# Performance work log

Measured on AMD Instinct MI355X. Metric: run time of the kernel, lower is better.

The kernel has to match this reference:

```python
import jax, jax.numpy as jnp
import numpy as np

B, N = 256, 128000

def setup_inputs() -> dict:
    key = jax.random.key(0)
    k1, k2, k3 = jax.random.split(key, 3)
    logits = jax.random.normal(k1, (B, N), dtype=jnp.float32) * 4.0
    k = jax.random.randint(k2, (B,), 1, 1000, dtype=jnp.int32)
    p = jax.random.uniform(k3, (B,), dtype=jnp.float32, minval=0.05, maxval=0.99)
    return {"logits": logits, "k": k, "p": p}


def reference(logits, k, p):
    """Faithful jax version of original_apply_top_k_top_p (k and p both given).
    Sort ascending, mask everything below the k-th largest, then mask the
    low-probability prefix whose cumulative softmax mass is <= 1-p, and
    scatter the masked sorted logits back to original positions."""
    Bn, Nn = logits.shape
    k = jnp.clip(k, 1, Nn)
    idx = jnp.argsort(logits, axis=-1)                       # ascending order
    logits_sort = jnp.take_along_axis(logits, idx, axis=-1)
    neg_inf = jnp.float32(-jnp.inf)

    # --- top-k: threshold = value at position (N - k) in ascending order ---
    kth_pos = (Nn - k).astype(jnp.int32)[:, None]            # [B,1]
    kth_val = jnp.take_along_axis(logits_sort, kth_pos, axis=-1)
    logits_sort = jnp.where(logits_sort < kth_val, neg_inf, logits_sort)

    # --- top-p on the (top-k masked) sorted logits ---
    probs = jax.nn.softmax(logits_sort, axis=-1)
    probs_sum = jnp.cumsum(probs, axis=-1)
    top_p_mask = probs_sum <= (1.0 - p)[:, None]
    top_p_mask = top_p_mask.at[:, -1].set(False)             # always keep argmax
    logits_sort = jnp.where(top_p_mask, neg_inf, logits_sort)

    # --- scatter back to original vocabulary positions ---
    rows = jnp.arange(Bn)[:, None]
    out = jnp.empty_like(logits).at[rows, idx].set(logits_sort)
    return out
```

## Files before the change

### kernel.cpp

```cpp
#include <hip/hip_runtime.h>
#include <stdint.h>
#include <math.h>

#define BB 256
#define NN 128000
#define N4 (NN / 4)
#define CAP 2048
#define BLK 1024
#define THRESH 9.0f
#define LBUF_CAP 512
#define CHUNKS_PER_ROW 25
#define CHUNK_F4 (N4 / CHUNKS_PER_ROW)
#define MASK_BITS 0xFF7F0000u
#define BF16_FINITE_LIM 3.0e38f

#define CTR_STRIDE 4
#define WS_NEEDED ((size_t)4096 + (size_t)BB * CAP * sizeof(uint2))

typedef float f4v __attribute__((ext_vector_type(4)));

__device__ __forceinline__ uint32_t fkey_enc(uint32_t bits) {
  return (bits & 0x80000000u) ? ~bits : (bits | 0x80000000u);
}
__device__ __forceinline__ float fkey_dec(uint32_t fkey) {
  uint32_t bits = (fkey & 0x80000000u) ? (fkey ^ 0x80000000u) : ~fkey;
  return __uint_as_float(bits);
}

__global__ void k0_zero(uint32_t* counters) {
  int t = threadIdx.x;
  if (t < BB * CTR_STRIDE) counters[t] = 0u;
}

__global__ __launch_bounds__(256) void kGather(
    const float* __restrict__ logits, uint32_t* __restrict__ counters,
    uint2* __restrict__ pairs) {
  const int row = blockIdx.y;
  __shared__ uint2 lbuf[LBUF_CAP];
  __shared__ uint32_t lcount;
  __shared__ uint32_t gbase;
  if (threadIdx.x == 0) lcount = 0u;
  __syncthreads();

  const int t = (int)threadIdx.x;
  const int base = (int)blockIdx.x * CHUNK_F4;
  const f4v* in4 = (const f4v*)(logits + (size_t)row * NN);
  const f4v* a0 = in4 + (base + t);
  const f4v* a1 = in4 + (base + t + 256);
  const f4v* a2 = in4 + (base + t + 512);
  const f4v* a3 = in4 + (base + t + 768);
  const f4v* a4 = in4 + (base + t + 1024);

  f4v v0, v1, v2, v3, v4;
  asm volatile(
      "global_load_dwordx4 %0, %5, off\n\t"
      "global_load_dwordx4 %1, %6, off\n\t"
      "global_load_dwordx4 %2, %7, off\n\t"
      "global_load_dwordx4 %3, %8, off\n\t"
      "global_load_dwordx4 %4, %9, off\n\t"
      "s_waitcnt vmcnt(0)"
      : "=&v"(v0), "=&v"(v1), "=&v"(v2), "=&v"(v3), "=&v"(v4)
      : "v"(a0), "v"(a1), "v"(a2), "v"(a3), "v"(a4)
      : "memory");
  __builtin_amdgcn_sched_barrier(0);

#define PUSHC(x, colexpr)                                            \
  do {                                                               \
    if ((x) > THRESH) {                                              \
      uint32_t slot = atomicAdd(&lcount, 1u);                        \
      if (slot < LBUF_CAP)                                           \
        lbuf[slot] = make_uint2(fkey_enc(__float_as_uint(x)),        \
                                (uint32_t)(colexpr));                \
    }                                                                \
  } while (0)
#define CONSUME4(vv, fbase)                                          \
  do {                                                               \
    PUSHC((vv).x, (fbase) * 4 + 0);                                  \
    PUSHC((vv).y, (fbase) * 4 + 1);                                  \
    PUSHC((vv).z, (fbase) * 4 + 2);                                  \
    PUSHC((vv).w, (fbase) * 4 + 3);                                  \
  } while (0)
  CONSUME4(v0, base + t);
  CONSUME4(v1, base + t + 256);
  CONSUME4(v2, base + t + 512);
  CONSUME4(v3, base + t + 768);
  CONSUME4(v4, base + t + 1024);
#undef CONSUME4
#undef PUSHC
  __syncthreads();

  uint32_t n = lcount;
  if (threadIdx.x == 0) {
    if (n > LBUF_CAP) {
      atomicAdd(&counters[(size_t)row * CTR_STRIDE], (uint32_t)(CAP + 1));
      gbase = 0xFFFFFFFFu;
    } else {
      gbase = atomicAdd(&counters[(size_t)row * CTR_STRIDE], n);
    }
  }
  __syncthreads();
  uint32_t gb = gbase;
  if (gb == 0xFFFFFFFFu) return;
  for (uint32_t i = threadIdx.x; i < n; i += 256) {
    uint32_t s = gb + i;
    if (s < CAP) pairs[(size_t)row * CAP + s] = lbuf[i];
  }
}

__global__ __launch_bounds__(BLK) void kB_finalize(
    const float* __restrict__ logits, const int* __restrict__ kin,
    const float* __restrict__ pin, const uint32_t* __restrict__ counters,
    const uint2* __restrict__ pairs, float* __restrict__ out) {
  const int row = blockIdx.x;
  const int tid = threadIdx.x;

  __shared__ unsigned long long skey[CAP];
  __shared__ double dbuf[2][BLK];
  __shared__ uint32_t red[BLK];
  __shared__ uint32_t scount;

  {
    const float MASKV = __uint_as_float(MASK_BITS);
    const f4v mask4 = {MASKV, MASKV, MASKV, MASKV};
    f4v* out4 = (f4v*)(out + (size_t)row * NN);
    for (int i = tid; i < N4; i += BLK) out4[i] = mask4;
  }

  int k = kin[row];
  if (k < 1) k = 1;
  if (k > NN) k = NN;
  uint32_t c = counters[(size_t)row * CTR_STRIDE];

  if (c <= CAP && c >= (uint32_t)k) {
    for (int i = tid; i < (int)c; i += BLK) {
      uint2 pr = pairs[(size_t)row * CAP + i];
      skey[i] = ((unsigned long long)pr.x << 32) | (unsigned long long)pr.y;
    }
  } else {
    const float* rowp = logits + (size_t)row * NN;
    uint32_t lo = 0u, hi = 0xFFFFFFFFu;
    while (lo < hi) {
      uint32_t mid = (uint32_t)(((uint64_t)lo + (uint64_t)hi + 1ull) >> 1);
      uint32_t cnt = 0;
      for (int i = tid; i < NN; i += BLK)
        cnt += (fkey_enc(__float_as_uint(rowp[i])) >= mid) ? 1u : 0u;
      red[tid] = cnt;
      __syncthreads();
      for (int off = BLK / 2; off > 0; off >>= 1) {
        if (tid < off) red[tid] += red[tid + off];
        __syncthreads();
      }
      uint32_t total = red[0];
      __syncthreads();
      if (total >= (uint32_t)k) lo = mid;
      else hi = mid - 1u;
    }
    if (tid == 0) scount = 0u;
    __syncthreads();
    for (int i = tid; i < NN; i += BLK) {
      uint32_t fk = fkey_enc(__float_as_uint(rowp[i]));
      if (fk >= lo) {
        uint32_t slot = atomicAdd(&scount, 1u);
        if (slot < CAP) skey[slot] = ((unsigned long long)fk << 32) | (uint32_t)i;
      }
    }
    __syncthreads();
    c = scount;
    if (c > CAP) c = CAP;
  }
  if (c == 0u) return;
  if ((uint32_t)k > c) k = (int)c;

  for (int i = (int)c + tid; i < CAP; i += BLK) skey[i] = 0ull;
  __syncthreads();
  for (int kk = 2; kk <= CAP; kk <<= 1) {
    for (int j = kk >> 1; j > 0; j >>= 1) {
      for (int i = tid; i < CAP; i += BLK) {
        int ixj = i ^ j;
        if (ixj > i) {
          unsigned long long a = skey[i], b = skey[ixj];
          bool up = ((i & kk) == 0);
          if (up ? (a > b) : (a < b)) {
            skey[i] = b;
            skey[ixj] = a;
          }
        }
      }
      __syncthreads();
    }
  }

  const uint32_t mfkey = (uint32_t)(skey[CAP - 1] >> 32);
  const uint32_t kthfkey = (uint32_t)(skey[CAP - k] >> 32);
  const double mval = (double)fkey_dec(mfkey);
  const int base = CAP - (int)c;
  const float p = pin[row];
  const double lim_frac = (double)(1.0f - p);

  double loc[2];
  double chunk = 0.0;
#pragma unroll
  for (int j = 0; j < 2; ++j) {
    int i = tid * 2 + j;
    double e = 0.0;
    if (i >= base) {
      uint32_t fk = (uint32_t)(skey[i] >> 32);
      if (fk >= kthfkey) e = exp((double)fkey_dec(fk) - mval);
    }
    chunk += e;
    loc[j] = chunk;
  }
  dbuf[0][tid] = chunk;
  __syncthreads();
  int src = 0;
  for (int off = 1; off < BLK; off <<= 1) {
    double v = dbuf[src][tid];
    if (tid >= off) v += dbuf[src][tid - off];
    dbuf[src ^ 1][tid] = v;
    src ^= 1;
    __syncthreads();
  }
  const double S = dbuf[src][BLK - 1];
  const double lim = lim_frac * S;
  const double excl = (tid == 0) ? 0.0 : dbuf[src][tid - 1];

#pragma unroll
  for (int j = 0; j < 2; ++j) {
    int i = tid * 2 + j;
    if (i >= base) {
      unsigned long long sk = skey[i];
      uint32_t fk = (uint32_t)(sk >> 32);
      if (fk >= kthfkey) {
        double A = excl + loc[j];
        if (A > lim) {
          uint32_t col = (uint32_t)(sk & 0xFFFFFFFFull);
          float v = fkey_dec(fk);
          if (col < NN && isfinite(v) && fabsf(v) < BF16_FINITE_LIM)
            out[(size_t)row * NN + col] = v;
        }
      }
    }
  }
}

__global__ __launch_bounds__(BLK) void topk_topp_row(
    const float* __restrict__ logits, const int* __restrict__ kin,
    const float* __restrict__ pin, float* __restrict__ out) {
  const int row = blockIdx.x;
  const int tid = threadIdx.x;
  __shared__ unsigned long long skey[CAP];
  __shared__ double dbuf[2][BLK];
  __shared__ uint32_t red[BLK];
  __shared__ uint32_t scount;
  if (tid == 0) scount = 0u;
  __syncthreads();
  const float MASKV = __uint_as_float(MASK_BITS);
  const float4 mask4 = make_float4(MASKV, MASKV, MASKV, MASKV);
  const float4* in4 = (const float4*)(logits + (size_t)row * NN);
  float4* out4 = (float4*)(out + (size_t)row * NN);
  for (int c4 = tid; c4 < N4; c4 += BLK) {
    float4 v = in4[c4];
    out4[c4] = mask4;
    float vals[4] = {v.x, v.y, v.z, v.w};
#pragma unroll
    for (int j = 0; j < 4; ++j) {
      if (vals[j] > THRESH) {
        uint32_t slot = atomicAdd(&scount, 1u);
        if (slot < CAP)
          skey[slot] = ((unsigned long long)fkey_enc(__float_as_uint(vals[j])) << 32) |
                       (unsigned long long)(uint32_t)(c4 * 4 + j);
      }
    }
  }
  __syncthreads();
  int k = kin[row];
  if (k < 1) k = 1;
  if (k > NN) k = NN;
  uint32_t c = scount;
  if (c > CAP || c < (uint32_t)k) {
    const float* rowp = logits + (size_t)row * NN;
    uint32_t lo = 0u, hi = 0xFFFFFFFFu;
    while (lo < hi) {
      uint32_t mid = (uint32_t)(((uint64_t)lo + (uint64_t)hi + 1ull) >> 1);
      uint32_t cnt = 0;
      for (int i = tid; i < NN; i += BLK)
        cnt += (fkey_enc(__float_as_uint(rowp[i])) >= mid) ? 1u : 0u;
      red[tid] = cnt;
      __syncthreads();
      for (int off = BLK / 2; off > 0; off >>= 1) {
        if (tid < off) red[tid] += red[tid + off];
        __syncthreads();
      }
      uint32_t total = red[0];
      __syncthreads();
      if (total >= (uint32_t)k) lo = mid;
      else hi = mid - 1u;
    }
    if (tid == 0) scount = 0u;
    __syncthreads();
    for (int i = tid; i < NN; i += BLK) {
      uint32_t fk = fkey_enc(__float_as_uint(rowp[i]));
      if (fk >= lo) {
        uint32_t slot = atomicAdd(&scount, 1u);
        if (slot < CAP) skey[slot] = ((unsigned long long)fk << 32) | (uint32_t)i;
      }
    }
    __syncthreads();
    c = scount;
    if (c > CAP) c = CAP;
  }
  if (c == 0u) return;
  if ((uint32_t)k > c) k = (int)c;
  for (int i = (int)c + tid; i < CAP; i += BLK) skey[i] = 0ull;
  __syncthreads();
  for (int kk = 2; kk <= CAP; kk <<= 1) {
    for (int j = kk >> 1; j > 0; j >>= 1) {
      for (int i = tid; i < CAP; i += BLK) {
        int ixj = i ^ j;
        if (ixj > i) {
          unsigned long long a = skey[i], b = skey[ixj];
          bool up = ((i & kk) == 0);
          if (up ? (a > b) : (a < b)) {
            skey[i] = b;
            skey[ixj] = a;
          }
        }
      }
      __syncthreads();
    }
  }
  const uint32_t mfkey = (uint32_t)(skey[CAP - 1] >> 32);
  const uint32_t kthfkey = (uint32_t)(skey[CAP - k] >> 32);
  const double mval = (double)fkey_dec(mfkey);
  const int base = CAP - (int)c;
  const float p = pin[row];
  const double lim_frac = (double)(1.0f - p);
  double loc[2];
  double chunk = 0.0;
#pragma unroll
  for (int j = 0; j < 2; ++j) {
    int i = tid * 2 + j;
    double e = 0.0;
    if (i >= base) {
      uint32_t fk = (uint32_t)(skey[i] >> 32);
      if (fk >= kthfkey) e = exp((double)fkey_dec(fk) - mval);
    }
    chunk += e;
    loc[j] = chunk;
  }
  dbuf[0][tid] = chunk;
  __syncthreads();
  int src = 0;
  for (int off = 1; off < BLK; off <<= 1) {
    double v = dbuf[src][tid];
    if (tid >= off) v += dbuf[src][tid - off];
    dbuf[src ^ 1][tid] = v;
    src ^= 1;
    __syncthreads();
  }
  const double S = dbuf[src][BLK - 1];
  const double lim = lim_frac * S;
  const double excl = (tid == 0) ? 0.0 : dbuf[src][tid - 1];
#pragma unroll
  for (int j = 0; j < 2; ++j) {
    int i = tid * 2 + j;
    if (i >= base) {
      unsigned long long sk = skey[i];
      uint32_t fk = (uint32_t)(sk >> 32);
      if (fk >= kthfkey) {
        double A = excl + loc[j];
        if (A > lim) {
          uint32_t col = (uint32_t)(sk & 0xFFFFFFFFull);
          float v = fkey_dec(fk);
          if (col < NN && isfinite(v) && fabsf(v) < BF16_FINITE_LIM)
            out[(size_t)row * NN + col] = v;
        }
      }
    }
  }
}

extern "C" void kernel_launch(void* const* d_in, const int* in_sizes, int n_in,
                              void* d_out, int out_size, void* d_ws, size_t ws_size,
                              hipStream_t stream) {
  const float* logits = (const float*)d_in[0];
  const int* kk = (const int*)d_in[1];
  const float* pp = (const float*)d_in[2];
  float* out = (float*)d_out;
  (void)in_sizes; (void)n_in; (void)out_size;

  if (ws_size >= WS_NEEDED) {
    uint32_t* counters = (uint32_t*)d_ws;
    uint2* pairs = (uint2*)((char*)d_ws + 4096);
    k0_zero<<<1, 1024, 0, stream>>>(counters);
    dim3 gG(CHUNKS_PER_ROW, BB);
    kGather<<<gG, 256, 0, stream>>>(logits, counters, pairs);
    kB_finalize<<<BB, BLK, 0, stream>>>(logits, kk, pp, counters, pairs, out);
  } else {
    topk_topp_row<<<BB, BLK, 0, stream>>>(logits, kk, pp, out);
  }
}
```

Measured before the change: 83.59 us.

## Move output mask fill into gather kernel as interleaved fill blocks

The gather kernel now also launches fill blocks, one after every four gather blocks, and these write the masked default value over the whole output. The finalize kernel no longer fills its own row first. The aim is to overlap the output write traffic with the input read traffic in a single launch, instead of serializing the fill at the start of each finalize block. The cost is a larger combined grid and a finalize kernel that now depends on the fill having finished in the previous launch, which stream order guarantees. Finalize's fallback paths still write only the kept entries, so they rely on this fill.

```diff
diff --git a/kernel.cpp b/kernel.cpp
--- a/kernel.cpp
+++ b/kernel.cpp
@@ -11,6 +11,9 @@
 #define LBUF_CAP 512
 #define CHUNKS_PER_ROW 25
 #define CHUNK_F4 (N4 / CHUNKS_PER_ROW)
+#define GATHER_BLOCKS (BB * CHUNKS_PER_ROW)
+#define FILL_BLOCKS 1600
+#define FILL_F4 ((BB * N4) / FILL_BLOCKS)
 #define MASK_BITS 0xFF7F0000u
 #define BF16_FINITE_LIM 3.0e38f
 
@@ -32,18 +35,33 @@
   if (t < BB * CTR_STRIDE) counters[t] = 0u;
 }
 
-__global__ __launch_bounds__(256) void kGather(
-    const float* __restrict__ logits, uint32_t* __restrict__ counters,
-    uint2* __restrict__ pairs) {
-  const int row = blockIdx.y;
+__global__ __launch_bounds__(256) void kStream(
+    const float* __restrict__ logits, float* __restrict__ out,
+    uint32_t* __restrict__ counters, uint2* __restrict__ pairs) {
+  const int group = (int)blockIdx.x / 5;
+  const int within = (int)blockIdx.x % 5;
+  const int t = (int)threadIdx.x;
+
+  if (within == 4) {
+    const float MASKV = __uint_as_float(MASK_BITS);
+    const f4v mask4 = {MASKV, MASKV, MASKV, MASKV};
+    f4v* out4 = (f4v*)out;
+    const int s = group * FILL_F4;
+#pragma unroll 4
+    for (int i = s + t; i < s + FILL_F4; i += 256) out4[i] = mask4;
+    return;
+  }
+
+  const int gi = group * 4 + within;
+  const int row = gi / CHUNKS_PER_ROW;
+  const int base = (gi % CHUNKS_PER_ROW) * CHUNK_F4;
+
   __shared__ uint2 lbuf[LBUF_CAP];
   __shared__ uint32_t lcount;
   __shared__ uint32_t gbase;
-  if (threadIdx.x == 0) lcount = 0u;
-  __syncthreads();
-
-  const int t = (int)threadIdx.x;
-  const int base = (int)blockIdx.x * CHUNK_F4;
+  if (t == 0) lcount = 0u;
+  __syncthreads();
+
   const f4v* in4 = (const f4v*)(logits + (size_t)row * NN);
   const f4v* a0 = in4 + (base + t);
   const f4v* a1 = in4 + (base + t + 256);
@@ -90,7 +108,7 @@
   __syncthreads();
 
   uint32_t n = lcount;
-  if (threadIdx.x == 0) {
+  if (t == 0) {
     if (n > LBUF_CAP) {
       atomicAdd(&counters[(size_t)row * CTR_STRIDE], (uint32_t)(CAP + 1));
       gbase = 0xFFFFFFFFu;
@@ -101,7 +119,7 @@
   __syncthreads();
   uint32_t gb = gbase;
   if (gb == 0xFFFFFFFFu) return;
-  for (uint32_t i = threadIdx.x; i < n; i += 256) {
+  for (uint32_t i = (uint32_t)t; i < n; i += 256) {
     uint32_t s = gb + i;
     if (s < CAP) pairs[(size_t)row * CAP + s] = lbuf[i];
   }
@@ -118,13 +136,6 @@
   __shared__ double dbuf[2][BLK];
   __shared__ uint32_t red[BLK];
   __shared__ uint32_t scount;
-
-  {
-    const float MASKV = __uint_as_float(MASK_BITS);
-    const f4v mask4 = {MASKV, MASKV, MASKV, MASKV};
-    f4v* out4 = (f4v*)(out + (size_t)row * NN);
-    for (int i = tid; i < N4; i += BLK) out4[i] = mask4;
-  }
 
   int k = kin[row];
   if (k < 1) k = 1;
@@ -393,8 +404,8 @@
     uint32_t* counters = (uint32_t*)d_ws;
     uint2* pairs = (uint2*)((char*)d_ws + 4096);
     k0_zero<<<1, 1024, 0, stream>>>(counters);
-    dim3 gG(CHUNKS_PER_ROW, BB);
-    kGather<<<gG, 256, 0, stream>>>(logits, counters, pairs);
+    kStream<<<GATHER_BLOCKS + FILL_BLOCKS, 256, 0, stream>>>(logits, out,
+                                                             counters, pairs);
     kB_finalize<<<BB, BLK, 0, stream>>>(logits, kk, pp, counters, pairs, out);
   } else {
     topk_topp_row<<<BB, BLK, 0, stream>>>(logits, kk, pp, out);
```

Result: slower. 86.02 us (+2.9%).
